# Performance work log

Measured on AMD Instinct MI355X. Metric: run time of the kernel, lower is better.

## Reference

```python
import jax, jax.numpy as jnp
import numpy as np
import math

B, C, TC, H, W = 8, 256, 512, 48, 48
EPS = 1e-6

def setup_inputs() -> dict:
    key = jax.random.key(0)
    kx, kt, kq, kk, kv = jax.random.split(key, 5)
    x = jax.random.normal(kx, (B, C, H, W), dtype=jnp.float32)
    token = jax.random.normal(kt, (B, TC, H, W), dtype=jnp.float32)
    # xavier_uniform for 1x1 conv weights [out, in]
    def xavier(k, fan_out, fan_in):
        a = math.sqrt(6.0 / (fan_in + fan_out))
        return jax.random.uniform(k, (fan_out, fan_in), dtype=jnp.float32, minval=-a, maxval=a)
    Wq = xavier(kq, C, C)
    Wk = xavier(kk, C, TC)
    Wv = xavier(kv, C, TC)
    alpha = jnp.float32(0.5)  # nonzero so the attention path affects the output
    return {"x": x, "token": token, "Wq": Wq, "Wk": Wk, "Wv": Wv, "alpha": alpha}

def reference(x, token, Wq, Wk, Wv, alpha):
    # 1x1 convs == per-pixel GEMMs over the channel dim
    q = jnp.einsum('oc,bchw->bohw', Wq, x)       # [B,C,H,W]
    k = jnp.einsum('oc,bchw->bohw', Wk, token)   # [B,C,H,W]
    v = jnp.einsum('oc,bchw->bohw', Wv, token)   # [B,C,H,W]
    b, c, h, w = q.shape
    n = h * w
    qf = q.reshape(b, c, n).transpose(0, 2, 1)   # [B,N,C]
    kf = k.reshape(b, c, n)                      # [B,C,N]
    vf = v.reshape(b, c, n).transpose(0, 2, 1)   # [B,N,C]
    # cosine normalization over the channel dim (F.normalize with eps clamp)
    qn = qf / jnp.maximum(jnp.linalg.norm(qf, axis=-1, keepdims=True), EPS)
    kn = kf / jnp.maximum(jnp.linalg.norm(kf, axis=1, keepdims=True), EPS)
    attn = jnp.einsum('bnc,bcm->bnm', qn, kn) / math.sqrt(c)  # [B,N,N]
    attn = jax.nn.softmax(attn, axis=-1)
    out = jnp.einsum('bnm,bmc->bnc', attn, vf)   # [B,N,C]
    out = out.transpose(0, 2, 1).reshape(b, c, h, w)
    return x + alpha * out
```

## Files before the change

kernel.cpp:

```cpp
#include <hip/hip_runtime.h>

#define B_   8
#define C_   256
#define TC_  512
#define HW_  2304
#define EPS_ 1e-6f
#define JS_  8
#define TPS_ 9

typedef __bf16 bf16_t;
typedef __bf16 bf16x8 __attribute__((ext_vector_type(8)));
typedef __bf16 bf16x4_t __attribute__((ext_vector_type(4)));
typedef float  f32x4 __attribute__((ext_vector_type(4)));
typedef unsigned int  u32;
typedef unsigned int  u32x4 __attribute__((ext_vector_type(4)));
typedef long long     i64;
typedef unsigned char u8;

__device__ __forceinline__ void g2l16(const void* g, void* l) {
    __builtin_amdgcn_global_load_lds(
        (const __attribute__((address_space(1))) unsigned int*)g,
        (__attribute__((address_space(3))) unsigned int*)l, 16, 0, 0);
}

__device__ __forceinline__ u8 to_fp8(float v) {
    return (u8)(__builtin_amdgcn_cvt_pk_fp8_f32(v, v, 0, false) & 0xff);
}

__global__ __launch_bounds__(256)
void wfrag_kernel(const float* __restrict__ wq, const float* __restrict__ wk,
                  const float* __restrict__ wv,
                  bf16_t* __restrict__ oq, bf16_t* __restrict__ ok,
                  bf16_t* __restrict__ ov)
{
    const int fid = blockIdx.x * 4 + (threadIdx.x >> 6);
    const int lane = threadIdx.x & 63;
    const int l16 = lane & 15, quad = lane >> 4;

    const float* src; bf16_t* dst; int cin, f;
    if (fid < 128)      { src = wq; dst = oq; cin = C_;  f = fid; }
    else if (fid < 384) { src = wk; dst = ok; cin = TC_; f = fid - 128; }
    else                { src = wv; dst = ov; cin = TC_; f = fid - 384; }
    const int nks = cin / 32;
    const int ot = f / nks, ks = f % nks;

    const float* s = src + (size_t)(ot * 16 + l16) * cin + ks * 32 + quad * 8;
    float4 a = *(const float4*)(s);
    float4 b = *(const float4*)(s + 4);
    bf16x8 o;
    o[0] = (__bf16)a.x; o[1] = (__bf16)a.y; o[2] = (__bf16)a.z; o[3] = (__bf16)a.w;
    o[4] = (__bf16)b.x; o[5] = (__bf16)b.y; o[6] = (__bf16)b.z; o[7] = (__bf16)b.w;
    *(bf16x8*)(dst + (size_t)f * 512 + lane * 8) = o;
}

template<int CIN, bool DO_V>
__global__ __launch_bounds__(256, 4)
void convqkv_kernel(const float* __restrict__ X, const bf16_t* __restrict__ Wa,
                    const bf16_t* __restrict__ Wvp, u8* __restrict__ outA,
                    u8* __restrict__ outV)
{
    const int bid = blockIdx.x;
    const int b  = bid & 7;
    const int n0 = (bid >> 3) * 16;
    const int tid = threadIdx.x;
    const int wv = tid >> 6;
    const int lane = tid & 63;
    const int quad = lane >> 4, l16 = lane & 15;
    const int NKS = CIN / 32;

    __shared__ bf16_t T[16][CIN + 8];
    __shared__ float ssp[4][16];

    {
        const float* Xb = X + (size_t)b * CIN * HW_ + n0;
        const int cl = tid >> 2;
        const int n4 = (tid & 3) * 4;
#pragma unroll
        for (int cp = 0; cp < CIN; cp += 64) {
            float4 v = *(const float4*)(Xb + (size_t)(cp + cl) * HW_ + n4);
            T[n4 + 0][cp + cl] = (__bf16)v.x;
            T[n4 + 1][cp + cl] = (__bf16)v.y;
            T[n4 + 2][cp + cl] = (__bf16)v.z;
            T[n4 + 3][cp + cl] = (__bf16)v.w;
        }
    }
    __syncthreads();

    bf16x8 af[CIN / 32];
#pragma unroll
    for (int ks = 0; ks < CIN / 32; ks++)
        af[ks] = *(const bf16x8*)(&T[l16][ks * 32 + quad * 8]);

    const int ot0 = wv * 4;

    f32x4 accK[4];
#pragma unroll
    for (int p = 0; p < 4; p++) accK[p] = (f32x4){0.f, 0.f, 0.f, 0.f};
    {
        const bf16_t* wbase = Wa + ((size_t)ot0 * NKS) * 512 + lane * 8;
#pragma unroll
        for (int ks = 0; ks < CIN / 32; ks++)
#pragma unroll
            for (int p = 0; p < 4; p++) {
                bf16x8 bw = *(const bf16x8*)(wbase + (size_t)(p * NKS + ks) * 512);
                accK[p] = __builtin_amdgcn_mfma_f32_16x16x32_bf16(af[ks], bw, accK[p], 0, 0, 0);
            }
    }

    {
        float ssr[4];
#pragma unroll
        for (int r = 0; r < 4; r++) {
            float ss = accK[0][r] * accK[0][r] + accK[1][r] * accK[1][r]
                     + accK[2][r] * accK[2][r] + accK[3][r] * accK[3][r];
            ss += __shfl_xor(ss, 1);
            ss += __shfl_xor(ss, 2);
            ss += __shfl_xor(ss, 4);
            ss += __shfl_xor(ss, 8);
            ssr[r] = ss;
        }
        if (l16 == 0) {
#pragma unroll
            for (int r = 0; r < 4; r++) ssp[wv][quad * 4 + r] = ssr[r];
        }
    }

    f32x4 accV[4];
    if (DO_V) {
#pragma unroll
        for (int p = 0; p < 4; p++) accV[p] = (f32x4){0.f, 0.f, 0.f, 0.f};
        const bf16_t* wbase = Wvp + ((size_t)ot0 * NKS) * 512 + lane * 8;
#pragma unroll
        for (int ks = 0; ks < CIN / 32; ks++)
#pragma unroll
            for (int p = 0; p < 4; p++) {
                bf16x8 aw = *(const bf16x8*)(wbase + (size_t)(p * NKS + ks) * 512);
                accV[p] = __builtin_amdgcn_mfma_f32_16x16x32_bf16(aw, af[ks], accV[p], 0, 0, 0);
            }
    }

    __syncthreads();

    float scale[4];
#pragma unroll
    for (int r = 0; r < 4; r++) {
        int px = quad * 4 + r;
        float s = ssp[0][px] + ssp[1][px] + ssp[2][px] + ssp[3][px];
        scale[r] = 1.0f / fmaxf(sqrtf(s), EPS_);
    }
    {
        u8* oa = outA + ((size_t)b * HW_ + n0 + quad * 4) * C_ + l16;
#pragma unroll
        for (int p = 0; p < 4; p++)
#pragma unroll
            for (int r = 0; r < 4; r++)
                oa[(size_t)r * C_ + (ot0 + p) * 16] = to_fp8(accK[p][r] * scale[r]);
    }

    if (DO_V) {
#pragma unroll
        for (int p = 0; p < 4; p++)
#pragma unroll
            for (int r = 0; r < 4; r++)
                outV[((size_t)b * C_ + (ot0 + p) * 16 + quad * 4 + r) * HW_ + n0 + l16]
                    = to_fp8(accV[p][r]);
    }
}

__global__ __launch_bounds__(256, 1)
void attn_part_kernel(const u8* __restrict__ q8, const u8* __restrict__ k8,
                      const u8* __restrict__ v8,
                      bf16_t* __restrict__ Opart, float* __restrict__ lpart)
{
    const int bid = blockIdx.x;
    const int b   = bid & 7;
    const int rr  = bid >> 3;
    const int js  = rr % JS_;
    const int mtb = rr / JS_;
    const int wv   = threadIdx.x >> 6;
    const int lane = threadIdx.x & 63;
    const int quad = lane >> 4;
    const int l16  = lane & 15;
    const int row0 = mtb * 128 + wv * 32;
    const int jbase = js * (TPS_ * 32);

    const u8* qb = q8 + (size_t)b * HW_ * C_;
    const u8* kb = k8 + (size_t)b * HW_ * C_;
    const u8* vb = v8 + (size_t)b * C_ * HW_;

    __shared__ u8 Kslab[TPS_ * 8192];
    __shared__ u8 Vslab[TPS_ * 8192];
    __shared__ u8 Psh[8 * 768];

    const int kj = lane & 31, kh = lane >> 5;
    const int vg = lane & 1,  vc = lane >> 1;
    for (int t = 0; t < 18; t++) {
        int ii = wv * 18 + t;
        int tt = ii >> 3, i = ii & 7;
        g2l16(kb + (size_t)(jbase + tt * 32 + kj) * C_ + (i * 2 + kh) * 16,
              Kslab + ii * 1024);
    }
    for (int t = 0; t < 18; t++) {
        int jj = wv * 18 + t;
        int tt = jj >> 3, i2 = jj & 7;
        g2l16(vb + (size_t)(i2 * 32 + vc) * HW_ + jbase + tt * 32 + vg * 16,
              Vslab + jj * 1024);
    }

    i64 aq0[8], aq1[8];
    {
        const u8* r0 = qb + (size_t)(row0 + l16) * C_ + quad * 8;
        const u8* r1 = r0 + 16 * C_;
#pragma unroll
        for (int t = 0; t < 8; t++) {
            aq0[t] = *(const i64*)(r0 + t * 32);
            aq1[t] = *(const i64*)(r1 + t * 32);
        }
    }

    f32x4 O[8][4];
#pragma unroll
    for (int m = 0; m < 8; m++)
#pragma unroll
        for (int c = 0; c < 4; c++) O[m][c] = (f32x4){0.f, 0.f, 0.f, 0.f};
    float lsum0[4] = {0.f, 0.f, 0.f, 0.f};
    float lsum1[4] = {0.f, 0.f, 0.f, 0.f};

    __syncthreads();

    u8* pw = Psh + wv * 1536;
    const int koff = (quad >> 1) * 512 + l16 * 16 + (quad & 1) * 8;
    const u32 sel = (quad < 2) ? 0x06040200u : 0x07050301u;
    const int vcol = (wv * 64 + l16) * 32 + quad * 8;

    for (int tt = 0; tt < TPS_; tt++) {
        const u8* Kb = Kslab + tt * 8192;
        const u8* Vb = Vslab + tt * 8192;

        f32x4 s00 = (f32x4){0.f,0.f,0.f,0.f}, s01 = (f32x4){0.f,0.f,0.f,0.f};
        f32x4 s10 = (f32x4){0.f,0.f,0.f,0.f}, s11 = (f32x4){0.f,0.f,0.f,0.f};
#pragma unroll
        for (int t = 0; t < 8; t++) {
            i64 bk0 = *(const i64*)(Kb + t * 1024 + koff);
            i64 bk1 = *(const i64*)(Kb + t * 1024 + koff + 256);
            s00 = __builtin_amdgcn_mfma_f32_16x16x32_fp8_fp8(aq0[t], bk0, s00, 0, 0, 0);
            s01 = __builtin_amdgcn_mfma_f32_16x16x32_fp8_fp8(aq0[t], bk1, s01, 0, 0, 0);
            s10 = __builtin_amdgcn_mfma_f32_16x16x32_fp8_fp8(aq1[t], bk0, s10, 0, 0, 0);
            s11 = __builtin_amdgcn_mfma_f32_16x16x32_fp8_fp8(aq1[t], bk1, s11, 0, 0, 0);
        }
#pragma unroll
        for (int r = 0; r < 4; r++) {
            float p00 = __expf(s00[r] * 0.0625f), p01 = __expf(s01[r] * 0.0625f);
            float p10 = __expf(s10[r] * 0.0625f), p11 = __expf(s11[r] * 0.0625f);
            lsum0[r] += p00 + p01;
            lsum1[r] += p10 + p11;
            u32 w0 = __builtin_amdgcn_cvt_pk_fp8_f32(p00, p01, 0, false);
            u32 w1 = __builtin_amdgcn_cvt_pk_fp8_f32(p10, p11, 0, false);
            int ro = (quad * 4 + r) * 48 + l16 * 2;
            *(short*)(pw + ro)       = (short)w0;
            *(short*)(pw + 768 + ro) = (short)w1;
        }
        __syncthreads();

        i64 ap[8];
#pragma unroll
        for (int mt = 0; mt < 8; mt++) {
            u32x4 d = *(const u32x4*)(Psh + mt * 768 + l16 * 48 + (quad & 1) * 16);
            u32 lo = __builtin_amdgcn_perm(d[1], d[0], sel);
            u32 hi = __builtin_amdgcn_perm(d[3], d[2], sel);
            ap[mt] = ((i64)hi << 32) | (i64)lo;
        }
        i64 bv[4];
#pragma unroll
        for (int ct = 0; ct < 4; ct++)
            bv[ct] = *(const i64*)(Vb + vcol + ct * 512);
#pragma unroll
        for (int mt = 0; mt < 8; mt++)
#pragma unroll
            for (int ct = 0; ct < 4; ct++)
                O[mt][ct] = __builtin_amdgcn_mfma_f32_16x16x32_fp8_fp8(ap[mt], bv[ct], O[mt][ct], 0, 0, 0);
        __syncthreads();
    }

#pragma unroll
    for (int r = 0; r < 4; r++) {
        float t0 = lsum0[r], t1 = lsum1[r];
        t0 += __shfl_xor(t0, 1); t0 += __shfl_xor(t0, 2);
        t0 += __shfl_xor(t0, 4); t0 += __shfl_xor(t0, 8);
        t1 += __shfl_xor(t1, 1); t1 += __shfl_xor(t1, 2);
        t1 += __shfl_xor(t1, 4); t1 += __shfl_xor(t1, 8);
        lsum0[r] = t0; lsum1[r] = t1;
    }
    float* lp = lpart + (size_t)(js * B_ + b) * HW_;
    if (l16 == 0) {
        float4 a0; a0.x = lsum0[0]; a0.y = lsum0[1]; a0.z = lsum0[2]; a0.w = lsum0[3];
        float4 a1; a1.x = lsum1[0]; a1.y = lsum1[1]; a1.z = lsum1[2]; a1.w = lsum1[3];
        *(float4*)(lp + row0 + quad * 4)      = a0;
        *(float4*)(lp + row0 + 16 + quad * 4) = a1;
    }

    bf16_t* op = Opart + (size_t)(js * B_ + b) * C_ * HW_;
#pragma unroll
    for (int mt = 0; mt < 8; mt++)
#pragma unroll
        for (int ct = 0; ct < 4; ct++) {
            int c = wv * 64 + ct * 16 + l16;
            bf16x4_t v0;
            v0[0] = (__bf16)O[mt][ct][0]; v0[1] = (__bf16)O[mt][ct][1];
            v0[2] = (__bf16)O[mt][ct][2]; v0[3] = (__bf16)O[mt][ct][3];
            *(bf16x4_t*)(op + (size_t)c * HW_ + mtb * 128 + mt * 16 + quad * 4) = v0;
        }
}

__global__ __launch_bounds__(256)
void epilogue_kernel(const float* __restrict__ x, const bf16_t* __restrict__ Opart,
                     const float* __restrict__ lpart, const float* __restrict__ alphaPtr,
                     float* __restrict__ out, int JS)
{
    const float a = *alphaPtr;
    const size_t S = (size_t)B_ * C_ * HW_;
    size_t flat = ((size_t)blockIdx.x * 256 + threadIdx.x) * 4;
    int bc = (int)(flat / HW_);
    int n  = (int)(flat % HW_);
    int b  = bc >> 8;
    float4 xv = *(const float4*)(x + flat);
    float s0 = 0.f, s1 = 0.f, s2 = 0.f, s3 = 0.f;
    float l0 = 0.f, l1 = 0.f, l2 = 0.f, l3 = 0.f;
    for (int js = 0; js < JS; js++) {
        bf16x4_t ov = *(const bf16x4_t*)(Opart + (size_t)js * S + flat);
        s0 += (float)ov[0]; s1 += (float)ov[1];
        s2 += (float)ov[2]; s3 += (float)ov[3];
        float4 lv = *(const float4*)(lpart + (size_t)(js * B_ + b) * HW_ + n);
        l0 += lv.x; l1 += lv.y; l2 += lv.z; l3 += lv.w;
    }
    float4 r;
    r.x = xv.x + a * s0 / l0;
    r.y = xv.y + a * s1 / l1;
    r.z = xv.z + a * s2 / l2;
    r.w = xv.w + a * s3 / l3;
    *(float4*)(out + flat) = r;
}

extern "C" void kernel_launch(void* const* d_in, const int* in_sizes, int n_in,
                              void* d_out, int out_size, void* d_ws, size_t ws_size,
                              hipStream_t stream)
{
    (void)in_sizes; (void)n_in; (void)out_size; (void)ws_size;
    const float* x     = (const float*)d_in[0];
    const float* token = (const float*)d_in[1];
    const float* Wq    = (const float*)d_in[2];
    const float* Wk    = (const float*)d_in[3];
    const float* Wv    = (const float*)d_in[4];
    const float* alpha = (const float*)d_in[5];
    float* out = (float*)d_out;

    const size_t S = (size_t)B_ * HW_ * C_;

    char* ws = (char*)d_ws;
    bf16_t* WqL   = (bf16_t*)(ws + 6 * S);
    bf16_t* WkL   = WqL + (size_t)C_ * C_;
    bf16_t* WvL   = WkL + (size_t)C_ * TC_;
    u8*     q8    = (u8*)(ws + 7 * S);
    u8*     k8    = (u8*)(ws + 8 * S);
    u8*     v8    = (u8*)(ws + 9 * S);
    bf16_t* Opart = (bf16_t*)(ws + 12 * S);
    float*  lpart = (float*)(ws + (12 + 2 * (size_t)JS_) * S);

    wfrag_kernel<<<dim3(160), dim3(256), 0, stream>>>(Wq, Wk, Wv, WqL, WkL, WvL);
    convqkv_kernel<C_,  false><<<dim3(B_ * HW_ / 16), dim3(256), 0, stream>>>(x,     WqL, nullptr, q8, nullptr);
    convqkv_kernel<TC_, true ><<<dim3(B_ * HW_ / 16), dim3(256), 0, stream>>>(token, WkL, WvL,     k8, v8);
    attn_part_kernel<<<dim3(JS_ * B_ * (HW_ / 128)), dim3(256), 0, stream>>>(q8, k8, v8, Opart, lpart);
    epilogue_kernel<<<dim3((int)(S / 1024)), dim3(256), 0, stream>>>(x, Opart, lpart, alpha, out, JS_);
}
```

Baseline: 264.5 us.

## Write K/V in MFMA fragment layout and stream from global without LDS

The K/V projection kernel now stores K and V in a pre-swizzled per-lane MFMA fragment layout, so the attention kernel can load operands straight from global memory with 16-byte vector loads. The attention kernel drops the LDS K/V slabs and the block-wide syncs. Each wave now owns a 16-row tile with all 256 output channels instead of 32 rows by 64 channels, and the grid doubles with 3 blocks per SM allowed. The aim is higher occupancy and no LDS staging or barriers, at the cost of each wave re-reading K/V from global/L2 rather than sharing it through LDS across the block.

Measured after the change: 298.3 us. 12.8% more time.

```diff
diff --git a/kernel.cpp b/kernel.cpp
--- a/kernel.cpp
+++ b/kernel.cpp
@@ -6,7 +6,6 @@
 #define HW_  2304
 #define EPS_ 1e-6f
 #define JS_  8
-#define TPS_ 9
 
 typedef __bf16 bf16_t;
 typedef __bf16 bf16x8 __attribute__((ext_vector_type(8)));
@@ -17,12 +16,6 @@
 typedef long long     i64;
 typedef unsigned char u8;
 
-__device__ __forceinline__ void g2l16(const void* g, void* l) {
-    __builtin_amdgcn_global_load_lds(
-        (const __attribute__((address_space(1))) unsigned int*)g,
-        (__attribute__((address_space(3))) unsigned int*)l, 16, 0, 0);
-}
-
 __device__ __forceinline__ u8 to_fp8(float v) {
     return (u8)(__builtin_amdgcn_cvt_pk_fp8_f32(v, v, 0, false) & 0xff);
 }
@@ -53,7 +46,7 @@
     *(bf16x8*)(dst + (size_t)f * 512 + lane * 8) = o;
 }
 
-template<int CIN, bool DO_V>
+template<int CIN, bool DO_V, bool FRAG_A>
 __global__ __launch_bounds__(256, 4)
 void convqkv_kernel(const float* __restrict__ X, const bf16_t* __restrict__ Wa,
                     const bf16_t* __restrict__ Wvp, u8* __restrict__ outA,
@@ -148,7 +141,17 @@
         float s = ssp[0][px] + ssp[1][px] + ssp[2][px] + ssp[3][px];
         scale[r] = 1.0f / fmaxf(sqrtf(s), EPS_);
     }
-    {
+
+    if (FRAG_A) {
+        u8* kfb = outA + (((size_t)b * 144 + (n0 >> 4)) * 4 + wv) * 1024;
+#pragma unroll
+        for (int p = 0; p < 4; p++)
+#pragma unroll
+            for (int r = 0; r < 4; r++) {
+                int lane_k = ((2 * p + (l16 >> 3)) & 3) * 16 + quad * 4 + r;
+                kfb[lane_k * 16 + (p >> 1) * 8 + (l16 & 7)] = to_fp8(accK[p][r] * scale[r]);
+            }
+    } else {
         u8* oa = outA + ((size_t)b * HW_ + n0 + quad * 4) * C_ + l16;
 #pragma unroll
         for (int p = 0; p < 4; p++)
@@ -158,158 +161,123 @@
     }
 
     if (DO_V) {
+        u8* vfb = outV + (((size_t)b * 72 + (n0 >> 5)) * 8 + wv * 2) * 1024;
+        const int quad_v = 2 * ((n0 >> 4) & 1) + (l16 >> 3);
 #pragma unroll
         for (int p = 0; p < 4; p++)
 #pragma unroll
-            for (int r = 0; r < 4; r++)
-                outV[((size_t)b * C_ + (ot0 + p) * 16 + quad * 4 + r) * HW_ + n0 + l16]
+            for (int r = 0; r < 4; r++) {
+                int lane_v = quad_v * 16 + quad * 4 + r;
+                vfb[(p >> 1) * 1024 + lane_v * 16 + (p & 1) * 8 + (l16 & 7)]
                     = to_fp8(accV[p][r]);
-    }
-}
-
-__global__ __launch_bounds__(256, 1)
-void attn_part_kernel(const u8* __restrict__ q8, const u8* __restrict__ k8,
-                      const u8* __restrict__ v8,
+            }
+    }
+}
+
+__global__ __launch_bounds__(256, 3)
+void attn_part_kernel(const u8* __restrict__ q8, const u8* __restrict__ kf,
+                      const u8* __restrict__ vf,
                       bf16_t* __restrict__ Opart, float* __restrict__ lpart)
 {
     const int bid = blockIdx.x;
     const int b   = bid & 7;
     const int rr  = bid >> 3;
-    const int js  = rr % JS_;
-    const int mtb = rr / JS_;
+    const int js  = rr & 7;
+    const int blk = rr >> 3;
     const int wv   = threadIdx.x >> 6;
     const int lane = threadIdx.x & 63;
     const int quad = lane >> 4;
     const int l16  = lane & 15;
-    const int row0 = mtb * 128 + wv * 32;
-    const int jbase = js * (TPS_ * 32);
-
-    const u8* qb = q8 + (size_t)b * HW_ * C_;
-    const u8* kb = k8 + (size_t)b * HW_ * C_;
-    const u8* vb = v8 + (size_t)b * C_ * HW_;
-
-    __shared__ u8 Kslab[TPS_ * 8192];
-    __shared__ u8 Vslab[TPS_ * 8192];
-    __shared__ u8 Psh[8 * 768];
-
-    const int kj = lane & 31, kh = lane >> 5;
-    const int vg = lane & 1,  vc = lane >> 1;
-    for (int t = 0; t < 18; t++) {
-        int ii = wv * 18 + t;
-        int tt = ii >> 3, i = ii & 7;
-        g2l16(kb + (size_t)(jbase + tt * 32 + kj) * C_ + (i * 2 + kh) * 16,
-              Kslab + ii * 1024);
-    }
-    for (int t = 0; t < 18; t++) {
-        int jj = wv * 18 + t;
-        int tt = jj >> 3, i2 = jj & 7;
-        g2l16(vb + (size_t)(i2 * 32 + vc) * HW_ + jbase + tt * 32 + vg * 16,
-              Vslab + jj * 1024);
-    }
-
-    i64 aq0[8], aq1[8];
+    const int row0 = (blk * 4 + wv) * 16;
+
+    __shared__ u8 Psh[4 * 768];
+    u8* pw = Psh + wv * 768;
+
+    i64 aq[8];
     {
-        const u8* r0 = qb + (size_t)(row0 + l16) * C_ + quad * 8;
-        const u8* r1 = r0 + 16 * C_;
-#pragma unroll
-        for (int t = 0; t < 8; t++) {
-            aq0[t] = *(const i64*)(r0 + t * 32);
-            aq1[t] = *(const i64*)(r1 + t * 32);
-        }
-    }
-
-    f32x4 O[8][4];
-#pragma unroll
-    for (int m = 0; m < 8; m++)
-#pragma unroll
-        for (int c = 0; c < 4; c++) O[m][c] = (f32x4){0.f, 0.f, 0.f, 0.f};
-    float lsum0[4] = {0.f, 0.f, 0.f, 0.f};
-    float lsum1[4] = {0.f, 0.f, 0.f, 0.f};
-
-    __syncthreads();
-
-    u8* pw = Psh + wv * 1536;
-    const int koff = (quad >> 1) * 512 + l16 * 16 + (quad & 1) * 8;
+        const u8* qr = q8 + (size_t)b * HW_ * C_ + (size_t)(row0 + l16) * C_ + quad * 8;
+#pragma unroll
+        for (int t = 0; t < 8; t++) aq[t] = *(const i64*)(qr + t * 32);
+    }
+
+    f32x4 O[16];
+#pragma unroll
+    for (int i = 0; i < 16; i++) O[i] = (f32x4){0.f, 0.f, 0.f, 0.f};
+    float lsum[4] = {0.f, 0.f, 0.f, 0.f};
+
+    const u8* kbase = kf + ((size_t)(b * 144 + js * 18) * 4) * 1024 + lane * 16;
+    const u8* vbase = vf + ((size_t)(b * 72  + js * 9 ) * 8) * 1024 + lane * 16;
     const u32 sel = (quad < 2) ? 0x06040200u : 0x07050301u;
-    const int vcol = (wv * 64 + l16) * 32 + quad * 8;
-
-    for (int tt = 0; tt < TPS_; tt++) {
-        const u8* Kb = Kslab + tt * 8192;
-        const u8* Vb = Vslab + tt * 8192;
-
-        f32x4 s00 = (f32x4){0.f,0.f,0.f,0.f}, s01 = (f32x4){0.f,0.f,0.f,0.f};
-        f32x4 s10 = (f32x4){0.f,0.f,0.f,0.f}, s11 = (f32x4){0.f,0.f,0.f,0.f};
-#pragma unroll
-        for (int t = 0; t < 8; t++) {
-            i64 bk0 = *(const i64*)(Kb + t * 1024 + koff);
-            i64 bk1 = *(const i64*)(Kb + t * 1024 + koff + 256);
-            s00 = __builtin_amdgcn_mfma_f32_16x16x32_fp8_fp8(aq0[t], bk0, s00, 0, 0, 0);
-            s01 = __builtin_amdgcn_mfma_f32_16x16x32_fp8_fp8(aq0[t], bk1, s01, 0, 0, 0);
-            s10 = __builtin_amdgcn_mfma_f32_16x16x32_fp8_fp8(aq1[t], bk0, s10, 0, 0, 0);
-            s11 = __builtin_amdgcn_mfma_f32_16x16x32_fp8_fp8(aq1[t], bk1, s11, 0, 0, 0);
-        }
+
+    for (int tt = 0; tt < 9; tt++) {
+        const u8* kb = kbase + (size_t)tt * 8192;
+        const u8* vb = vbase + (size_t)tt * 8192;
+
+        u32x4 kd[8];
+#pragma unroll
+        for (int i = 0; i < 8; i++) kd[i] = *(const u32x4*)(kb + i * 1024);
+        f32x4 s0 = (f32x4){0.f,0.f,0.f,0.f}, s1 = (f32x4){0.f,0.f,0.f,0.f};
+#pragma unroll
+        for (int p = 0; p < 4; p++) {
+            i64 b00 = (i64)kd[p][0]     | ((i64)kd[p][1]     << 32);
+            i64 b01 = (i64)kd[p][2]     | ((i64)kd[p][3]     << 32);
+            i64 b10 = (i64)kd[4 + p][0] | ((i64)kd[4 + p][1] << 32);
+            i64 b11 = (i64)kd[4 + p][2] | ((i64)kd[4 + p][3] << 32);
+            s0 = __builtin_amdgcn_mfma_f32_16x16x32_fp8_fp8(aq[2 * p],     b00, s0, 0, 0, 0);
+            s0 = __builtin_amdgcn_mfma_f32_16x16x32_fp8_fp8(aq[2 * p + 1], b01, s0, 0, 0, 0);
+            s1 = __builtin_amdgcn_mfma_f32_16x16x32_fp8_fp8(aq[2 * p],     b10, s1, 0, 0, 0);
+            s1 = __builtin_amdgcn_mfma_f32_16x16x32_fp8_fp8(aq[2 * p + 1], b11, s1, 0, 0, 0);
+        }
+
 #pragma unroll
         for (int r = 0; r < 4; r++) {
-            float p00 = __expf(s00[r] * 0.0625f), p01 = __expf(s01[r] * 0.0625f);
-            float p10 = __expf(s10[r] * 0.0625f), p11 = __expf(s11[r] * 0.0625f);
-            lsum0[r] += p00 + p01;
-            lsum1[r] += p10 + p11;
-            u32 w0 = __builtin_amdgcn_cvt_pk_fp8_f32(p00, p01, 0, false);
-            u32 w1 = __builtin_amdgcn_cvt_pk_fp8_f32(p10, p11, 0, false);
-            int ro = (quad * 4 + r) * 48 + l16 * 2;
-            *(short*)(pw + ro)       = (short)w0;
-            *(short*)(pw + 768 + ro) = (short)w1;
-        }
-        __syncthreads();
-
-        i64 ap[8];
-#pragma unroll
-        for (int mt = 0; mt < 8; mt++) {
-            u32x4 d = *(const u32x4*)(Psh + mt * 768 + l16 * 48 + (quad & 1) * 16);
+            float p0 = __expf(s0[r] * 0.0625f), p1 = __expf(s1[r] * 0.0625f);
+            lsum[r] += p0 + p1;
+            u32 w = __builtin_amdgcn_cvt_pk_fp8_f32(p0, p1, 0, false);
+            *(short*)(pw + (quad * 4 + r) * 48 + l16 * 2) = (short)w;
+        }
+        i64 ap;
+        {
+            u32x4 d = *(const u32x4*)(pw + l16 * 48 + (quad & 1) * 16);
             u32 lo = __builtin_amdgcn_perm(d[1], d[0], sel);
             u32 hi = __builtin_amdgcn_perm(d[3], d[2], sel);
-            ap[mt] = ((i64)hi << 32) | (i64)lo;
-        }
-        i64 bv[4];
-#pragma unroll
-        for (int ct = 0; ct < 4; ct++)
-            bv[ct] = *(const i64*)(Vb + vcol + ct * 512);
-#pragma unroll
-        for (int mt = 0; mt < 8; mt++)
-#pragma unroll
-            for (int ct = 0; ct < 4; ct++)
-                O[mt][ct] = __builtin_amdgcn_mfma_f32_16x16x32_fp8_fp8(ap[mt], bv[ct], O[mt][ct], 0, 0, 0);
-        __syncthreads();
+            ap = ((i64)hi << 32) | (i64)lo;
+        }
+
+        u32x4 vd[8];
+#pragma unroll
+        for (int u = 0; u < 8; u++) vd[u] = *(const u32x4*)(vb + u * 1024);
+#pragma unroll
+        for (int u = 0; u < 8; u++) {
+            i64 bv0 = (i64)vd[u][0] | ((i64)vd[u][1] << 32);
+            i64 bv1 = (i64)vd[u][2] | ((i64)vd[u][3] << 32);
+            O[2 * u]     = __builtin_amdgcn_mfma_f32_16x16x32_fp8_fp8(ap, bv0, O[2 * u],     0, 0, 0);
+            O[2 * u + 1] = __builtin_amdgcn_mfma_f32_16x16x32_fp8_fp8(ap, bv1, O[2 * u + 1], 0, 0, 0);
+        }
     }
 
 #pragma unroll
     for (int r = 0; r < 4; r++) {
-        float t0 = lsum0[r], t1 = lsum1[r];
+        float t0 = lsum[r];
         t0 += __shfl_xor(t0, 1); t0 += __shfl_xor(t0, 2);
         t0 += __shfl_xor(t0, 4); t0 += __shfl_xor(t0, 8);
-        t1 += __shfl_xor(t1, 1); t1 += __shfl_xor(t1, 2);
-        t1 += __shfl_xor(t1, 4); t1 += __shfl_xor(t1, 8);
-        lsum0[r] = t0; lsum1[r] = t1;
+        lsum[r] = t0;
     }
     float* lp = lpart + (size_t)(js * B_ + b) * HW_;
     if (l16 == 0) {
-        float4 a0; a0.x = lsum0[0]; a0.y = lsum0[1]; a0.z = lsum0[2]; a0.w = lsum0[3];
-        float4 a1; a1.x = lsum1[0]; a1.y = lsum1[1]; a1.z = lsum1[2]; a1.w = lsum1[3];
-        *(float4*)(lp + row0 + quad * 4)      = a0;
-        *(float4*)(lp + row0 + 16 + quad * 4) = a1;
+        float4 a0; a0.x = lsum[0]; a0.y = lsum[1]; a0.z = lsum[2]; a0.w = lsum[3];
+        *(float4*)(lp + row0 + quad * 4) = a0;
     }
 
     bf16_t* op = Opart + (size_t)(js * B_ + b) * C_ * HW_;
 #pragma unroll
-    for (int mt = 0; mt < 8; mt++)
-#pragma unroll
-        for (int ct = 0; ct < 4; ct++) {
-            int c = wv * 64 + ct * 16 + l16;
-            bf16x4_t v0;
-            v0[0] = (__bf16)O[mt][ct][0]; v0[1] = (__bf16)O[mt][ct][1];
-            v0[2] = (__bf16)O[mt][ct][2]; v0[3] = (__bf16)O[mt][ct][3];
-            *(bf16x4_t*)(op + (size_t)c * HW_ + mtb * 128 + mt * 16 + quad * 4) = v0;
-        }
+    for (int ct = 0; ct < 16; ct++) {
+        int c = ct * 16 + l16;
+        bf16x4_t v0;
+        v0[0] = (__bf16)O[ct][0]; v0[1] = (__bf16)O[ct][1];
+        v0[2] = (__bf16)O[ct][2]; v0[3] = (__bf16)O[ct][3];
+        *(bf16x4_t*)(op + (size_t)c * HW_ + row0 + quad * 4) = v0;
+    }
 }
 
 __global__ __launch_bounds__(256)
@@ -361,14 +329,14 @@
     bf16_t* WkL   = WqL + (size_t)C_ * C_;
     bf16_t* WvL   = WkL + (size_t)C_ * TC_;
     u8*     q8    = (u8*)(ws + 7 * S);
-    u8*     k8    = (u8*)(ws + 8 * S);
-    u8*     v8    = (u8*)(ws + 9 * S);
+    u8*     kf    = (u8*)(ws + 8 * S);
+    u8*     vf    = (u8*)(ws + 9 * S);
     bf16_t* Opart = (bf16_t*)(ws + 12 * S);
     float*  lpart = (float*)(ws + (12 + 2 * (size_t)JS_) * S);
 
     wfrag_kernel<<<dim3(160), dim3(256), 0, stream>>>(Wq, Wk, Wv, WqL, WkL, WvL);
-    convqkv_kernel<C_,  false><<<dim3(B_ * HW_ / 16), dim3(256), 0, stream>>>(x,     WqL, nullptr, q8, nullptr);
-    convqkv_kernel<TC_, true ><<<dim3(B_ * HW_ / 16), dim3(256), 0, stream>>>(token, WkL, WvL,     k8, v8);
-    attn_part_kernel<<<dim3(JS_ * B_ * (HW_ / 128)), dim3(256), 0, stream>>>(q8, k8, v8, Opart, lpart);
+    convqkv_kernel<C_,  false, false><<<dim3(B_ * HW_ / 16), dim3(256), 0, stream>>>(x,     WqL, nullptr, q8, nullptr);
+    convqkv_kernel<TC_, true,  true ><<<dim3(B_ * HW_ / 16), dim3(256), 0, stream>>>(token, WkL, WvL,     kf, vf);
+    attn_part_kernel<<<dim3(JS_ * B_ * (HW_ / 64)), dim3(256), 0, stream>>>(q8, kf, vf, Opart, lpart);
     epilogue_kernel<<<dim3((int)(S / 1024)), dim3(256), 0, stream>>>(x, Opart, lpart, alpha, out, JS_);
 }
```
